# Optimization experiments

Measured on AMD Instinct MI355X. Metric: run time of the kernel, lower is better.

Reference implementation:

```python
import jax, jax.numpy as jnp
import numpy as np

B, LQ, LK, C = 16, 1024, 1024, 512
WH = int(LQ ** 0.5)  # 32


def setup_inputs() -> dict:
    key = jax.random.key(0)
    ks = jax.random.split(key, 6)
    s1 = 1.0 / np.sqrt(LK)
    return {
        "query": jax.random.normal(ks[0], (B, LQ, C), jnp.float32),
        "key": jax.random.normal(ks[1], (B, LK, C), jnp.float32),
        "value": jax.random.normal(ks[2], (B, LK, C), jnp.float32),
        # nn.Linear weights, stored [out_features, in_features] like torch
        "w1": jax.random.normal(ks[3], (LK, LK), jnp.float32) * s1,
        "w2": jax.random.normal(ks[4], (LK, LK), jnp.float32) * s1,
        "w3": jax.random.normal(ks[5], (1, LK), jnp.float32) * s1,
    }


def reference(query, key, value, w1, w2, w3):
    # cosine-similarity matrix (computed under no_grad in the original)
    q = query / 100.0
    k = key / 100.0
    qn = jnp.sqrt(jnp.sum(q * q, axis=-1))[:, :, None]   # [B, LQ, 1]
    kn = jnp.sqrt(jnp.sum(k * k, axis=-1))[:, None, :]   # [B, 1, LK]
    outer = qn * kn                                       # rank-1 outer product [B, LQ, LK]
    upper = jnp.einsum('bqc,bkc->bqk', q, k)              # [B, LQ, LK]
    similar_rev = jax.lax.stop_gradient(upper / (outer + 1e-6))

    # 3-layer MLP gating over the LK axis -> scalar weight per query row
    h = jax.nn.gelu(jnp.einsum('bqk,ok->bqo', similar_rev, w1), approximate=False)
    h = jax.nn.gelu(jnp.einsum('bqk,ok->bqo', h, w2), approximate=False)
    w = jnp.einsum('bqk,ok->bqo', h, w3)[..., 0]          # [B, LQ]

    # weight^T @ similar_rev / wh, then tanh -> per-key scalar gate [B, LK, 1]
    weight = jnp.einsum('bq,bqk->bk', w, similar_rev) / WH
    weight = jnp.tanh(weight)[:, :, None]

    # value modulation + residual
    return value * weight + value
```

## Files before the change

kernel.cpp:

```cpp
#include <hip/hip_runtime.h>
#include <hip/hip_bf16.h>

#define B_  16
#define LQ_ 1024
#define LK_ 1024
#define C_  512

typedef __attribute__((ext_vector_type(4))) float f32x4;
typedef __attribute__((ext_vector_type(8))) short bf16x8;

__device__ __forceinline__ float bf2f(ushort u) {
  union { unsigned int i; float f; } v; v.i = ((unsigned int)u) << 16; return v.f;
}
__device__ __forceinline__ ushort f2bf(float f) {
  union { float f; unsigned int i; } v; v.f = f;
  unsigned int r = v.i + 0x7fffu + ((v.i >> 16) & 1u);
  return (ushort)(r >> 16);
}
__device__ __forceinline__ float gelu_exact(float x) {
  return 0.5f * x * (1.0f + erff(x * 0.70710678118654752f));
}

__device__ __forceinline__ void gload_lds16(const ushort* g, ushort* l) {
  __builtin_amdgcn_global_load_lds(
      (const __attribute__((address_space(1))) void*)g,
      (__attribute__((address_space(3))) void*)l, 16, 0, 0);
}

__global__ __launch_bounds__(256) void prep_qk(const float* __restrict__ x,
                                               ushort* __restrict__ xb,
                                               float* __restrict__ norms) {
  int wid = blockIdx.x * 4 + (threadIdx.x >> 6);
  int lane = threadIdx.x & 63;
  const float* xr = x + (long)wid * C_;
  ushort* xo = xb + (long)wid * C_;
  float ss = 0.f;
#pragma unroll
  for (int i0 = 0; i0 < 2; ++i0) {
    int i = lane * 4 + i0 * 256;
    float4 v = *(const float4*)(xr + i);
    ss += v.x * v.x + v.y * v.y + v.z * v.z + v.w * v.w;
    ushort4 o;
    o.x = f2bf(v.x); o.y = f2bf(v.y); o.z = f2bf(v.z); o.w = f2bf(v.w);
    *(ushort4*)(xo + i) = o;
  }
#pragma unroll
  for (int off = 32; off > 0; off >>= 1) ss += __shfl_xor(ss, off);
  if (lane == 0) norms[wid] = sqrtf(ss);
}

__global__ __launch_bounds__(256) void conv_bf16(const float* __restrict__ x,
                                                 ushort* __restrict__ o, int n4) {
  int i = blockIdx.x * 256 + threadIdx.x;
  if (i < n4) {
    float4 v = *(const float4*)(x + (long)i * 4);
    ushort4 u;
    u.x = f2bf(v.x); u.y = f2bf(v.y); u.z = f2bf(v.z); u.w = f2bf(v.w);
    *(ushort4*)(o + (long)i * 4) = u;
  }
}

template <int EPI>
__global__ __launch_bounds__(512, 2) void gemm256(
    const ushort* __restrict__ A, const ushort* __restrict__ Bm,
    ushort* __restrict__ Cc, int K, long sA, long sB, long sC,
    const float* __restrict__ qn, const float* __restrict__ kn,
    const float* __restrict__ w3v, float* __restrict__ wv) {
  int per = (int)(gridDim.x >> 3);
  int orig = blockIdx.x;
  int id = (orig & 7) * per + (orig >> 3);
  int b = id >> 4;
  int rt = id & 15;
  const int bm = (rt >> 2) * 256, bn = (rt & 3) * 256;

  A += (long)b * sA + (long)bm * K;
  Bm += (long)b * sB;

  __shared__ ushort At[2][256 * 64];
  __shared__ ushort Bt[2][256 * 64];

  const int tid = threadIdx.x;
  const int lane = tid & 63, w = tid >> 6;
  const int wr = w >> 2, wc = w & 3;
  const int l16 = lane & 15, lhi = lane >> 4;

  f32x4 acc[8][4] = {};

  const ushort* gAs[4];
  const ushort* gBs[4];
  int dstc[4];
#pragma unroll
  for (int s = 0; s < 4; ++s) {
    int c = s * 512 + tid;
    int l = c >> 3;
    int cb = (c & 7) ^ (l & 7);
    gAs[s] = A + (long)l * K + cb * 8;
    int nh = l >> 7, wcb = (l >> 5) & 3, jj = l & 31;
    int rb = wcb * 64 + nh * 32 + jj;
    gBs[s] = Bm + (long)(bn + rb) * K + cb * 8;
    dstc[s] = (s * 512 + (tid & ~63)) * 8;
  }

  {
    ushort* Ad = &At[0][0];
    ushort* Bd = &Bt[0][0];
    gload_lds16(gAs[0], Ad + dstc[0]);
    gload_lds16(gAs[2], Ad + dstc[2]);
    gload_lds16(gBs[0], Bd + dstc[0]);
    gload_lds16(gBs[1], Bd + dstc[1]);
    gload_lds16(gBs[2], Bd + dstc[2]);
    gload_lds16(gBs[3], Bd + dstc[3]);
    gload_lds16(gAs[1], Ad + dstc[1]);
    gload_lds16(gAs[3], Ad + dstc[3]);
  }
  asm volatile("s_waitcnt vmcnt(4)" ::: "memory");
  __builtin_amdgcn_s_barrier();

  const int xk0 = (lhi ^ (l16 & 7)) * 8;
  const int xk1 = ((4 + lhi) ^ (l16 & 7)) * 8;

#define MFMA_QUAD(MH, NH, BB)                                              \
  __builtin_amdgcn_s_setprio(1);                                           \
  _Pragma("unroll") for (int mi = 0; mi < 4; ++mi)                         \
      _Pragma("unroll") for (int ni = 0; ni < 2; ++ni)                     \
          _Pragma("unroll") for (int kk = 0; kk < 2; ++kk)                 \
              acc[(MH)*4 + mi][(NH)*2 + ni] =                              \
      __builtin_amdgcn_mfma_f32_16x16x32_bf16(                             \
          aa[mi][kk], BB[ni][kk], acc[(MH)*4 + mi][(NH)*2 + ni], 0, 0, 0); \
  __builtin_amdgcn_s_setprio(0);

  const int nt = K / 64;
  int cur = 0;
  for (int t = 0; t < nt; ++t) {
    const ushort* Ac = &At[cur][0];
    const ushort* Bc = &Bt[cur][0];
    ushort* Ad = &At[cur ^ 1][0];
    ushort* Bd = &Bt[cur ^ 1][0];
    const int ko = (t + 1) * 64;
    const bool pf = (t + 1 < nt);

    bf16x8 aa[4][2], b0[2][2], b1[2][2];

#pragma unroll
    for (int mi = 0; mi < 4; ++mi) {
      int r = wr * 128 + mi * 16 + l16;
      aa[mi][0] = *(const bf16x8*)(Ac + r * 64 + xk0);
      aa[mi][1] = *(const bf16x8*)(Ac + r * 64 + xk1);
    }
#pragma unroll
    for (int ni = 0; ni < 2; ++ni) {
      int lb = wc * 32 + ni * 16 + l16;
      b0[ni][0] = *(const bf16x8*)(Bc + lb * 64 + xk0);
      b0[ni][1] = *(const bf16x8*)(Bc + lb * 64 + xk1);
    }
    if (pf) {
      gload_lds16(gAs[0] + ko, Ad + dstc[0]);
      gload_lds16(gAs[2] + ko, Ad + dstc[2]);
      asm volatile("s_waitcnt vmcnt(4)" ::: "memory");
    } else {
      asm volatile("s_waitcnt vmcnt(2)" ::: "memory");
    }
    __builtin_amdgcn_s_barrier();
    asm volatile("s_waitcnt lgkmcnt(0)" ::: "memory");
    __builtin_amdgcn_sched_barrier(0);
    MFMA_QUAD(0, 0, b0)

#pragma unroll
    for (int ni = 0; ni < 2; ++ni) {
      int lb = 128 + wc * 32 + ni * 16 + l16;
      b1[ni][0] = *(const bf16x8*)(Bc + lb * 64 + xk0);
      b1[ni][1] = *(const bf16x8*)(Bc + lb * 64 + xk1);
    }
    if (pf) {
      gload_lds16(gBs[0] + ko, Bd + dstc[0]);
      gload_lds16(gBs[1] + ko, Bd + dstc[1]);
      asm volatile("s_waitcnt vmcnt(4)" ::: "memory");
    } else {
      asm volatile("s_waitcnt vmcnt(0)" ::: "memory");
    }
    __builtin_amdgcn_s_barrier();
    asm volatile("s_waitcnt lgkmcnt(0)" ::: "memory");
    __builtin_amdgcn_sched_barrier(0);
    MFMA_QUAD(0, 1, b1)

#pragma unroll
    for (int mi = 0; mi < 4; ++mi) {
      int r = wr * 128 + 64 + mi * 16 + l16;
      aa[mi][0] = *(const bf16x8*)(Ac + r * 64 + xk0);
      aa[mi][1] = *(const bf16x8*)(Ac + r * 64 + xk1);
    }
    if (pf) {
      gload_lds16(gBs[2] + ko, Bd + dstc[2]);
      gload_lds16(gBs[3] + ko, Bd + dstc[3]);
      asm volatile("s_waitcnt vmcnt(4)" ::: "memory");
    }
    __builtin_amdgcn_s_barrier();
    asm volatile("s_waitcnt lgkmcnt(0)" ::: "memory");
    __builtin_amdgcn_sched_barrier(0);
    MFMA_QUAD(1, 0, b0)

    if (pf) {
      gload_lds16(gAs[1] + ko, Ad + dstc[1]);
      gload_lds16(gAs[3] + ko, Ad + dstc[3]);
      asm volatile("s_waitcnt vmcnt(4)" ::: "memory");
    }
    __builtin_amdgcn_s_barrier();
    MFMA_QUAD(1, 1, b1)

    cur ^= 1;
  }
#undef MFMA_QUAD

  if constexpr (EPI == 2) {
    float* wvb = wv + (long)b * LQ_;
    float w3c[4];
#pragma unroll
    for (int n = 0; n < 4; ++n) w3c[n] = w3v[bn + wc * 64 + n * 16 + l16];
#pragma unroll
    for (int m = 0; m < 8; ++m)
#pragma unroll
      for (int rr = 0; rr < 4; ++rr) {
        float s = 0.f;
#pragma unroll
        for (int n = 0; n < 4; ++n)
          s += gelu_exact(acc[m][n][rr]) * w3c[n];
        s += __shfl_xor(s, 1);
        s += __shfl_xor(s, 2);
        s += __shfl_xor(s, 4);
        s += __shfl_xor(s, 8);
        if (l16 == 0)
          atomicAdd(&wvb[bm + wr * 128 + m * 16 + lhi * 4 + rr], s);
      }
  } else {
    Cc += (long)b * sC;
    const float* qnb = qn + (long)b * LQ_;
    const float* knb = kn + (long)b * LK_;
#pragma unroll
    for (int m = 0; m < 8; ++m) {
      int row0 = bm + wr * 128 + m * 16 + lhi * 4;
#pragma unroll
      for (int n = 0; n < 4; ++n) {
        int col = bn + wc * 64 + n * 16 + l16;
#pragma unroll
        for (int rr = 0; rr < 4; ++rr) {
          float v = acc[m][n][rr];
          int grow = row0 + rr;
          if (EPI == 0) {
            v = v / (qnb[grow] * knb[col] + 1e-2f);
          } else {
            v = gelu_exact(v);
          }
          Cc[(long)grow * 1024 + col] = f2bf(v);
        }
      }
    }
  }
}

__global__ __launch_bounds__(256) void gate_partial(const ushort* __restrict__ S,
                                                    const float* __restrict__ wv,
                                                    float* __restrict__ wraw) {
  int b = blockIdx.z;
  int k = blockIdx.x * 256 + threadIdx.x;
  int q0 = blockIdx.y * 128;
  const ushort* Sb = S + (long)b * LQ_ * LK_;
  const float* wb = wv + b * LQ_;
  float acc = 0.f;
#pragma unroll 4
  for (int q = q0; q < q0 + 128; ++q) acc += wb[q] * bf2f(Sb[(long)q * LK_ + k]);
  atomicAdd(&wraw[b * LK_ + k], acc);
}

__global__ __launch_bounds__(256) void finalize(const float* __restrict__ value,
                                                const float* __restrict__ wraw,
                                                float* __restrict__ out) {
  long i = (long)blockIdx.x * 256 + threadIdx.x;
  long e = i * 4;
  int row = (int)(e >> 9);
  float g = 1.f + tanhf(wraw[row] * (1.f / 32.f));
  float4 v = ((const float4*)value)[i];
  v.x *= g; v.y *= g; v.z *= g; v.w *= g;
  ((float4*)out)[i] = v;
}

extern "C" void kernel_launch(void* const* d_in, const int* in_sizes, int n_in,
                              void* d_out, int out_size, void* d_ws,
                              size_t ws_size, hipStream_t stream) {
  const float* query = (const float*)d_in[0];
  const float* key   = (const float*)d_in[1];
  const float* value = (const float*)d_in[2];
  const float* w1    = (const float*)d_in[3];
  const float* w2    = (const float*)d_in[4];
  const float* w3    = (const float*)d_in[5];
  float* out = (float*)d_out;

  const size_t QB_BYTES = (size_t)B_ * LQ_ * C_ * 2;
  const size_t S_BYTES  = (size_t)B_ * LQ_ * LK_ * 2;
  const size_t W_BYTES  = (size_t)LK_ * LK_ * 2;
  const size_t OFF_QB = 0;
  const size_t OFF_KB = OFF_QB + QB_BYTES;
  const size_t OFF_S  = OFF_KB + QB_BYTES;
  const size_t OFF_H1 = OFF_S + S_BYTES;
  const size_t OFF_W1 = OFF_H1 + S_BYTES;
  const size_t OFF_W2 = OFF_W1 + W_BYTES;
  const size_t OFF_QN = OFF_W2 + W_BYTES;
  const size_t OFF_KN = OFF_QN + (size_t)B_ * LQ_ * 4;
  const size_t OFF_WV = OFF_KN + (size_t)B_ * LK_ * 4;
  const size_t OFF_WR = OFF_WV + (size_t)B_ * LQ_ * 4;
  const size_t TOTAL  = OFF_WR + (size_t)B_ * LK_ * 4;
  if (ws_size < TOTAL) return;

  char* ws = (char*)d_ws;
  ushort* Qb  = (ushort*)(ws + OFF_QB);
  ushort* Kb  = (ushort*)(ws + OFF_KB);
  ushort* S   = (ushort*)(ws + OFF_S);
  ushort* h1  = (ushort*)(ws + OFF_H1);
  ushort* W1b = (ushort*)(ws + OFF_W1);
  ushort* W2b = (ushort*)(ws + OFF_W2);
  float* qn   = (float*)(ws + OFF_QN);
  float* kn   = (float*)(ws + OFF_KN);
  float* wv   = (float*)(ws + OFF_WV);
  float* wraw = (float*)(ws + OFF_WR);

  prep_qk<<<dim3(B_ * LQ_ / 4), 256, 0, stream>>>(query, Qb, qn);
  prep_qk<<<dim3(B_ * LK_ / 4), 256, 0, stream>>>(key, Kb, kn);
  conv_bf16<<<dim3(LK_ * LK_ / 4 / 256), 256, 0, stream>>>(w1, W1b, LK_ * LK_ / 4);
  conv_bf16<<<dim3(LK_ * LK_ / 4 / 256), 256, 0, stream>>>(w2, W2b, LK_ * LK_ / 4);
  hipMemsetAsync(wraw, 0, (size_t)B_ * LK_ * 4, stream);
  hipMemsetAsync(wv, 0, (size_t)B_ * LQ_ * 4, stream);

  gemm256<0><<<dim3(256), 512, 0, stream>>>(
      Qb, Kb, S, C_, (long)LQ_ * C_, (long)LK_ * C_, (long)LQ_ * LK_,
      qn, kn, nullptr, nullptr);

  gemm256<1><<<dim3(256), 512, 0, stream>>>(
      S, W1b, h1, LK_, (long)LQ_ * LK_, 0L, (long)LQ_ * LK_,
      nullptr, nullptr, nullptr, nullptr);

  gemm256<2><<<dim3(256), 512, 0, stream>>>(
      h1, W2b, nullptr, LK_, (long)LQ_ * LK_, 0L, 0L,
      nullptr, nullptr, w3, wv);

  gate_partial<<<dim3(LK_ / 256, LQ_ / 128, B_), 256, 0, stream>>>(S, wv, wraw);

  finalize<<<dim3((size_t)B_ * LK_ * C_ / 4 / 256), 256, 0, stream>>>(value, wraw, out);
}
```

Baseline: 166.2 us.

## Double-buffer LDS fragments in registers to overlap reads with MFMA

```diff
diff --git a/kernel.cpp b/kernel.cpp
--- a/kernel.cpp
+++ b/kernel.cpp
@@ -26,6 +26,9 @@
       (const __attribute__((address_space(1))) void*)g,
       (__attribute__((address_space(3))) void*)l, 16, 0, 0);
 }
+
+#define VMCNT(n) asm volatile("s_waitcnt vmcnt(" #n ")" ::: "memory")
+#define BARRIER() asm volatile("s_barrier" ::: "memory")
 
 __global__ __launch_bounds__(256) void prep_qk(const float* __restrict__ x,
                                                ushort* __restrict__ xb,
@@ -104,29 +107,40 @@
   {
     ushort* Ad = &At[0][0];
     ushort* Bd = &Bt[0][0];
-    gload_lds16(gAs[0], Ad + dstc[0]);
-    gload_lds16(gAs[2], Ad + dstc[2]);
-    gload_lds16(gBs[0], Bd + dstc[0]);
-    gload_lds16(gBs[1], Bd + dstc[1]);
-    gload_lds16(gBs[2], Bd + dstc[2]);
-    gload_lds16(gBs[3], Bd + dstc[3]);
-    gload_lds16(gAs[1], Ad + dstc[1]);
-    gload_lds16(gAs[3], Ad + dstc[3]);
-  }
-  asm volatile("s_waitcnt vmcnt(4)" ::: "memory");
-  __builtin_amdgcn_s_barrier();
+#pragma unroll
+    for (int s = 0; s < 4; ++s) {
+      gload_lds16(gAs[s], Ad + dstc[s]);
+      gload_lds16(gBs[s], Bd + dstc[s]);
+    }
+  }
+  VMCNT(0);
+  BARRIER();
 
   const int xk0 = (lhi ^ (l16 & 7)) * 8;
   const int xk1 = ((4 + lhi) ^ (l16 & 7)) * 8;
 
-#define MFMA_QUAD(MH, NH, BB)                                              \
+  bf16x8 aaA[4][2], aaB[4][2], bA[2][2], bB[2][2];
+#pragma unroll
+  for (int mi = 0; mi < 4; ++mi) {
+    int r = wr * 128 + mi * 16 + l16;
+    aaA[mi][0] = *(const bf16x8*)(&At[0][0] + r * 64 + xk0);
+    aaA[mi][1] = *(const bf16x8*)(&At[0][0] + r * 64 + xk1);
+  }
+#pragma unroll
+  for (int ni = 0; ni < 2; ++ni) {
+    int lb = wc * 32 + ni * 16 + l16;
+    bA[ni][0] = *(const bf16x8*)(&Bt[0][0] + lb * 64 + xk0);
+    bA[ni][1] = *(const bf16x8*)(&Bt[0][0] + lb * 64 + xk1);
+  }
+
+#define MFMA_QUAD(MH, NH, AA, BB)                                          \
   __builtin_amdgcn_s_setprio(1);                                           \
   _Pragma("unroll") for (int mi = 0; mi < 4; ++mi)                         \
       _Pragma("unroll") for (int ni = 0; ni < 2; ++ni)                     \
           _Pragma("unroll") for (int kk = 0; kk < 2; ++kk)                 \
               acc[(MH)*4 + mi][(NH)*2 + ni] =                              \
       __builtin_amdgcn_mfma_f32_16x16x32_bf16(                             \
-          aa[mi][kk], BB[ni][kk], acc[(MH)*4 + mi][(NH)*2 + ni], 0, 0, 0); \
+          AA[mi][kk], BB[ni][kk], acc[(MH)*4 + mi][(NH)*2 + ni], 0, 0, 0); \
   __builtin_amdgcn_s_setprio(0);
 
   const int nt = K / 64;
@@ -139,73 +153,66 @@
     const int ko = (t + 1) * 64;
     const bool pf = (t + 1 < nt);
 
-    bf16x8 aa[4][2], b0[2][2], b1[2][2];
-
-#pragma unroll
-    for (int mi = 0; mi < 4; ++mi) {
-      int r = wr * 128 + mi * 16 + l16;
-      aa[mi][0] = *(const bf16x8*)(Ac + r * 64 + xk0);
-      aa[mi][1] = *(const bf16x8*)(Ac + r * 64 + xk1);
-    }
-#pragma unroll
-    for (int ni = 0; ni < 2; ++ni) {
-      int lb = wc * 32 + ni * 16 + l16;
-      b0[ni][0] = *(const bf16x8*)(Bc + lb * 64 + xk0);
-      b0[ni][1] = *(const bf16x8*)(Bc + lb * 64 + xk1);
-    }
     if (pf) {
       gload_lds16(gAs[0] + ko, Ad + dstc[0]);
       gload_lds16(gAs[2] + ko, Ad + dstc[2]);
-      asm volatile("s_waitcnt vmcnt(4)" ::: "memory");
+      VMCNT(2);
     } else {
-      asm volatile("s_waitcnt vmcnt(2)" ::: "memory");
-    }
-    __builtin_amdgcn_s_barrier();
-    asm volatile("s_waitcnt lgkmcnt(0)" ::: "memory");
-    __builtin_amdgcn_sched_barrier(0);
-    MFMA_QUAD(0, 0, b0)
-
+      VMCNT(0);
+    }
+    BARRIER();
 #pragma unroll
     for (int ni = 0; ni < 2; ++ni) {
       int lb = 128 + wc * 32 + ni * 16 + l16;
-      b1[ni][0] = *(const bf16x8*)(Bc + lb * 64 + xk0);
-      b1[ni][1] = *(const bf16x8*)(Bc + lb * 64 + xk1);
-    }
+      bB[ni][0] = *(const bf16x8*)(Bc + lb * 64 + xk0);
+      bB[ni][1] = *(const bf16x8*)(Bc + lb * 64 + xk1);
+    }
+    MFMA_QUAD(0, 0, aaA, bA)
+
     if (pf) {
       gload_lds16(gBs[0] + ko, Bd + dstc[0]);
       gload_lds16(gBs[1] + ko, Bd + dstc[1]);
-      asm volatile("s_waitcnt vmcnt(4)" ::: "memory");
-    } else {
-      asm volatile("s_waitcnt vmcnt(0)" ::: "memory");
-    }
-    __builtin_amdgcn_s_barrier();
-    asm volatile("s_waitcnt lgkmcnt(0)" ::: "memory");
-    __builtin_amdgcn_sched_barrier(0);
-    MFMA_QUAD(0, 1, b1)
-
+    }
+    BARRIER();
 #pragma unroll
     for (int mi = 0; mi < 4; ++mi) {
       int r = wr * 128 + 64 + mi * 16 + l16;
-      aa[mi][0] = *(const bf16x8*)(Ac + r * 64 + xk0);
-      aa[mi][1] = *(const bf16x8*)(Ac + r * 64 + xk1);
-    }
+      aaB[mi][0] = *(const bf16x8*)(Ac + r * 64 + xk0);
+      aaB[mi][1] = *(const bf16x8*)(Ac + r * 64 + xk1);
+    }
+    MFMA_QUAD(0, 1, aaA, bB)
+
+    if (pf) {
+      gload_lds16(gAs[1] + ko, Ad + dstc[1]);
+      gload_lds16(gAs[3] + ko, Ad + dstc[3]);
+      VMCNT(4);
+    }
+    BARRIER();
+    if (pf) {
+#pragma unroll
+      for (int mi = 0; mi < 4; ++mi) {
+        int r = wr * 128 + mi * 16 + l16;
+        aaA[mi][0] = *(const bf16x8*)(Ad + r * 64 + xk0);
+        aaA[mi][1] = *(const bf16x8*)(Ad + r * 64 + xk1);
+      }
+    }
+    MFMA_QUAD(1, 0, aaB, bA)
+
     if (pf) {
       gload_lds16(gBs[2] + ko, Bd + dstc[2]);
       gload_lds16(gBs[3] + ko, Bd + dstc[3]);
-      asm volatile("s_waitcnt vmcnt(4)" ::: "memory");
-    }
-    __builtin_amdgcn_s_barrier();
-    asm volatile("s_waitcnt lgkmcnt(0)" ::: "memory");
-    __builtin_amdgcn_sched_barrier(0);
-    MFMA_QUAD(1, 0, b0)
-
-    if (pf) {
-      gload_lds16(gAs[1] + ko, Ad + dstc[1]);
-      gload_lds16(gAs[3] + ko, Ad + dstc[3]);
-      asm volatile("s_waitcnt vmcnt(4)" ::: "memory");
-    }
-    __builtin_amdgcn_s_barrier();
-    MFMA_QUAD(1, 1, b1)
+      VMCNT(4);
+    }
+    BARRIER();
+    if (pf) {
+#pragma unroll
+      for (int ni = 0; ni < 2; ++ni) {
+        int lb = wc * 32 + ni * 16 + l16;
+        bA[ni][0] = *(const bf16x8*)(Bd + lb * 64 + xk0);
+        bA[ni][1] = *(const bf16x8*)(Bd + lb * 64 + xk1);
+      }
+    }
+    MFMA_QUAD(1, 1, aaB, bB)
 
     cur ^= 1;
   }
```

Measured after the change: 178.4 us. 1.07x slower.
